# Kernel tuning notes

Measured on AMD Instinct MI355X. Metric: run time of the kernel, lower is better.

Reference implementation:

```python
import jax, jax.numpy as jnp
import numpy as np

EMB = 1024
HEADS = 16
HEAD_DIM = EMB // HEADS
EPS = 1e-5


def gelu_tanh(x):
    c = jnp.sqrt(jnp.asarray(2.0 / jnp.pi, x.dtype))
    return 0.5 * x * (1.0 + jnp.tanh(c * (x + 0.044715 * x ** 3)))


def layernorm(x, scale, shift):
    mean = jnp.mean(x, axis=-1, keepdims=True)
    var = jnp.mean((x - mean) ** 2, axis=-1, keepdims=True)  # unbiased=False
    return scale * (x - mean) / jnp.sqrt(var + EPS) + shift


def setup_inputs() -> dict:
    key = jax.random.key(0)
    ks = jax.random.split(key, 12)
    d, dff = EMB, 4 * EMB
    sd = 1.0 / np.sqrt(d)
    inp = {
        "x": jax.random.normal(ks[0], (2, 2048, d), jnp.float32),
        "Wq": jax.random.normal(ks[1], (d, d), jnp.float32) * sd,
        "Wk": jax.random.normal(ks[2], (d, d), jnp.float32) * sd,
        "Wv": jax.random.normal(ks[3], (d, d), jnp.float32) * sd,
        "Wo": jax.random.normal(ks[4], (d, d), jnp.float32) * sd,
        "bo": jnp.zeros((d,), jnp.float32),
        "W1": jax.random.normal(ks[5], (d, dff), jnp.float32) * sd,
        "b1": jnp.zeros((dff,), jnp.float32),
        "W2": jax.random.normal(ks[6], (dff, d), jnp.float32) * (1.0 / np.sqrt(dff)),
        "b2": jnp.zeros((d,), jnp.float32),
        "g1": jnp.ones((d,), jnp.float32),
        "s1": jnp.zeros((d,), jnp.float32),
        "g2": jnp.ones((d,), jnp.float32),
        "s2": jnp.zeros((d,), jnp.float32),
    }
    return inp


def attention(x, Wq, Wk, Wv, Wo, bo):
    b, s, d = x.shape
    def heads(W):
        return (x @ W).reshape(b, s, HEADS, HEAD_DIM).transpose(0, 2, 1, 3)  # b h s hd
    q, k, v = heads(Wq), heads(Wk), heads(Wv)
    scores = jnp.einsum("bhqd,bhkd->bhqk", q, k)
    causal = jnp.tril(jnp.ones((s, s), bool))
    scores = jnp.where(causal, scores, -jnp.inf)
    w = jax.nn.softmax(scores / np.sqrt(HEAD_DIM), axis=-1)
    ctx = jnp.einsum("bhqk,bhkd->bqhd", w, v).reshape(b, s, d)
    return ctx @ Wo + bo


def reference(x, Wq, Wk, Wv, Wo, bo, W1, b1, W2, b2, g1, s1, g2, s2):
    h = x + attention(layernorm(x, g1, s1), Wq, Wk, Wv, Wo, bo)
    y = layernorm(h, g2, s2)
    y = gelu_tanh(y @ W1 + b1) @ W2 + b2
    return h + y
```

## Files before the change

kernel.cpp:

```cpp
#include <hip/hip_runtime.h>
#include <hip/hip_bf16.h>
#include <stdint.h>
#include <math.h>

#define EMB   1024
#define DFF   4096
#define HEADS 16
#define HD    64
#define BATCH 2
#define SEQ   2048
#define ROWS  (BATCH * SEQ)

typedef __hip_bfloat16 bf16;
typedef short bf16x8_t __attribute__((ext_vector_type(8)));
typedef float f32x4_t __attribute__((ext_vector_type(4)));

typedef const uint32_t __attribute__((address_space(1)))* gp_t;
typedef uint32_t __attribute__((address_space(3)))* lp_t;

__device__ __forceinline__ void async_copy16(const bf16* g, short* l) {
    __builtin_amdgcn_global_load_lds((gp_t)(const void*)g, (lp_t)(void*)l, 16, 0, 0);
}

__device__ __forceinline__ void wait_lds() {
    __asm__ volatile("" ::: "memory");
    __builtin_amdgcn_s_waitcnt(0xC07F);
    __asm__ volatile("" ::: "memory");
}

__device__ __forceinline__ float gelu_f(float x) {
    float z = 0.7978845608028654f * (x + 0.044715f * x * x * x);
    float e = __builtin_amdgcn_exp2f(z * 2.885390081777927f);
    float t = 1.0f - 2.0f * __builtin_amdgcn_rcpf(e + 1.0f);
    return 0.5f * x * (1.0f + t);
}

__device__ __forceinline__ short bf16_bits(float x) {
    bf16 b = (bf16)x;
    short s;
    __builtin_memcpy(&s, &b, 2);
    return s;
}

__device__ __forceinline__ bf16x8_t load8(const bf16* p) {
    bf16x8_t v;
    __builtin_memcpy(&v, p, 16);
    return v;
}

template<int EPI, int BM>
__global__ __launch_bounds__(256) void gemm_k(
    const bf16* __restrict__ A, const bf16* __restrict__ BT,
    bf16* __restrict__ outB, float* __restrict__ outF,
    const float* __restrict__ bias, const float* __restrict__ resF,
    int N, int K, size_t bStrideZ, size_t cStrideZ)
{
    __shared__ alignas(16) short As[2][BM * 32];
    __shared__ alignas(16) short Bs[2][128 * 32];
    constexpr int AI  = BM / 32;
    constexpr int AIS = BM / 64;
    const int tid  = threadIdx.x;
    const int wave = tid >> 6;
    const int lane = tid & 63;
    const int quad = lane >> 4;
    const int l16  = lane & 15;
    const int m0 = blockIdx.y * BM;
    const int n0 = blockIdx.x * 128;
    const int wm = (wave >> 1) * (BM / 2);
    const int wn = (wave & 1) * 64;

    const bf16* Bz = BT + (size_t)blockIdx.z * bStrideZ;

    const bf16* Ag[AIS]; int aoff[AIS];
    const bf16* Bg[2];   int boff[2];
    #pragma unroll
    for (int i = 0; i < AIS; i++) {
        const int c = i * 256 + tid;
        const int row = c >> 2;
        const int lch = (c & 3) ^ ((row >> 1) & 3);
        Ag[i]   = A + (size_t)(m0 + row) * K + lch * 8;
        aoff[i] = (i * 256 + wave * 64) * 8;
    }
    #pragma unroll
    for (int i = 0; i < 2; i++) {
        const int c = i * 256 + tid;
        const int row = c >> 2;
        const int lch = (c & 3) ^ ((row >> 1) & 3);
        Bg[i]   = Bz + (size_t)(n0 + row) * K + lch * 8;
        boff[i] = (i * 256 + wave * 64) * 8;
    }

    f32x4_t acc[AI][4] = {};

    #pragma unroll
    for (int i = 0; i < AIS; i++) async_copy16(Ag[i], &As[0][aoff[i]]);
    #pragma unroll
    for (int i = 0; i < 2; i++)   async_copy16(Bg[i], &Bs[0][boff[i]]);
    __syncthreads();

    int cur = 0;
    for (int k0 = 0; k0 < K; k0 += 32) {
        const int kn = k0 + 32;
        if (kn < K) {
            #pragma unroll
            for (int i = 0; i < AIS; i++) async_copy16(Ag[i] + kn, &As[cur ^ 1][aoff[i]]);
            #pragma unroll
            for (int i = 0; i < 2; i++)   async_copy16(Bg[i] + kn, &Bs[cur ^ 1][boff[i]]);
        }
        bf16x8_t a[AI], b[4];
        #pragma unroll
        for (int i = 0; i < AI; i++) {
            const int r = wm + i * 16 + l16;
            a[i] = *(const bf16x8_t*)&As[cur][r * 32 + ((quad ^ ((r >> 1) & 3)) << 3)];
        }
        #pragma unroll
        for (int j = 0; j < 4; j++) {
            const int r = wn + j * 16 + l16;
            b[j] = *(const bf16x8_t*)&Bs[cur][r * 32 + ((quad ^ ((r >> 1) & 3)) << 3)];
        }
        #pragma unroll
        for (int i = 0; i < AI; i++)
            #pragma unroll
            for (int j = 0; j < 4; j++)
                acc[i][j] = __builtin_amdgcn_mfma_f32_16x16x32_bf16(
                    a[i], b[j], acc[i][j], 0, 0, 0);
        __syncthreads();
        cur ^= 1;
    }

    bf16* outBz = (EPI == 0) ? outB + (size_t)blockIdx.z * cStrideZ : outB;
    #pragma unroll
    for (int j = 0; j < 4; j++) {
        const int col = n0 + wn + j * 16 + l16;
        float bv = 0.0f;
        if constexpr (EPI != 0) bv = bias[col];
        #pragma unroll
        for (int i = 0; i < AI; i++) {
            #pragma unroll
            for (int r = 0; r < 4; r++) {
                const int row = m0 + wm + i * 16 + quad * 4 + r;
                float v = acc[i][j][r] + bv;
                if constexpr (EPI == 1 || EPI == 3) {
                    v += resF[(size_t)row * N + col];
                    outF[(size_t)row * N + col] = v;
                } else if constexpr (EPI == 2) {
                    outBz[(size_t)row * N + col] = (bf16)gelu_f(v);
                } else {
                    outBz[(size_t)row * N + col] = (bf16)v;
                }
            }
        }
    }
}

__global__ __launch_bounds__(256) void ln_k(
    const float* __restrict__ x, const float* __restrict__ g,
    const float* __restrict__ s, bf16* __restrict__ out)
{
    const int row = blockIdx.x;
    const int t = threadIdx.x;
    const size_t base = (size_t)row * EMB + t * 4;
    float v[4];
    #pragma unroll
    for (int e = 0; e < 4; e++) v[e] = x[base + e];
    float sum = v[0] + v[1] + v[2] + v[3];
    float sq  = v[0]*v[0] + v[1]*v[1] + v[2]*v[2] + v[3]*v[3];
    #pragma unroll
    for (int o = 1; o < 64; o <<= 1) {
        sum += __shfl_xor(sum, o);
        sq  += __shfl_xor(sq, o);
    }
    __shared__ float ssum[4], ssq[4];
    const int wave = t >> 6;
    if ((t & 63) == 0) { ssum[wave] = sum; ssq[wave] = sq; }
    __syncthreads();
    sum = ssum[0] + ssum[1] + ssum[2] + ssum[3];
    sq  = ssq[0] + ssq[1] + ssq[2] + ssq[3];
    const float mean = sum * (1.0f / EMB);
    const float var  = sq * (1.0f / EMB) - mean * mean;
    const float rstd = rsqrtf(var + 1e-5f);
    #pragma unroll
    for (int e = 0; e < 4; e++)
        out[base + e] = (bf16)(g[t * 4 + e] * (v[e] - mean) * rstd + s[t * 4 + e]);
}

template<typename T>
__global__ __launch_bounds__(256) void transpose_k(
    const T* __restrict__ src, bf16* __restrict__ dst, int R, int C)
{
    __shared__ bf16 tile[64][65];
    const size_t bo = (size_t)blockIdx.z * R * C;
    const int tx = threadIdx.x, ty = threadIdx.y;
    const int r0 = blockIdx.y * 64, c0 = blockIdx.x * 64;
    #pragma unroll
    for (int i = 0; i < 16; i++) {
        int r = ty + i * 4;
        tile[r][tx] = (bf16)(float)src[bo + (size_t)(r0 + r) * C + c0 + tx];
    }
    __syncthreads();
    #pragma unroll
    for (int i = 0; i < 16; i++) {
        int c = ty + i * 4;
        dst[bo + (size_t)(c0 + c) * R + r0 + tx] = tile[tx][c];
    }
}

__global__ __launch_bounds__(256) void transpose3_k(
    const float* __restrict__ s0, const float* __restrict__ s1,
    const float* __restrict__ s2, bf16* __restrict__ dst, int R, int C)
{
    __shared__ bf16 tile[64][65];
    const float* src = blockIdx.z == 0 ? s0 : (blockIdx.z == 1 ? s1 : s2);
    bf16* d = dst + (size_t)blockIdx.z * R * C;
    const int tx = threadIdx.x, ty = threadIdx.y;
    const int r0 = blockIdx.y * 64, c0 = blockIdx.x * 64;
    #pragma unroll
    for (int i = 0; i < 16; i++) {
        int r = ty + i * 4;
        tile[r][tx] = (bf16)src[(size_t)(r0 + r) * C + c0 + tx];
    }
    __syncthreads();
    #pragma unroll
    for (int i = 0; i < 16; i++) {
        int c = ty + i * 4;
        d[(size_t)(c0 + c) * R + r0 + tx] = tile[tx][c];
    }
}

__global__ __launch_bounds__(256) void attn_k(
    const bf16* __restrict__ q, const bf16* __restrict__ k,
    const bf16* __restrict__ vt, bf16* __restrict__ ctx)
{
    __shared__ alignas(16) short Ks[2][32 * 64];
    __shared__ alignas(16) short Vs[2][64 * 32];
    __shared__ alignas(16) short P[4][16 * 40];
    const int tid = threadIdx.x;
    const int wv = tid >> 6;
    const int lane = tid & 63;
    const int quad = lane >> 4, l16 = lane & 15;

    const int fid = (int)blockIdx.x;
    const int lid = (fid & 7) * 128 + (fid >> 3);
    const int chunk = 31 - (lid & 31);
    const int h = (lid >> 5) & 15;
    const int b = lid >> 9;
    const size_t rowBase = (size_t)b * SEQ;
    const int qb   = chunk * 64 + wv * 16;
    const int nkbw = ((qb + 15) >> 5) + 1;
    const int NK   = chunk * 2 + 2;

    const bf16* kcol  = k + rowBase * EMB + h * HD;
    const bf16* vbase = vt + (size_t)(b * HEADS + h) * HD * SEQ;

    bf16x8_t aq[2];
    #pragma unroll
    for (int s2 = 0; s2 < 2; s2++)
        aq[s2] = load8(&q[(rowBase + qb + l16) * EMB + h * HD + s2 * 32 + quad * 8]);

    f32x4_t O[4] = {};
    float l_p[4] = {};

    const int krow = tid >> 3;
    const int kcc  = (tid & 7) ^ (krow & 7);
    const int vrow = tid >> 2;
    const int vcc  = (tid & 3) ^ (vrow & 3) ^ ((vrow >> 2) & 3);

    async_copy16(kcol + (size_t)krow * EMB + kcc * 8, &Ks[0][wv * 512]);
    async_copy16(vbase + (size_t)vrow * SEQ + vcc * 8, &Vs[0][wv * 512]);
    __syncthreads();

    constexpr float SC = 0.125f * 1.44269504088896f;

    int cur = 0;
    for (int kb = 0; kb < NK; ++kb) {
        const int kbase = kb * 32;
        if (kb + 1 < NK) {
            const int nb = kbase + 32;
            async_copy16(kcol + (size_t)(nb + krow) * EMB + kcc * 8, &Ks[cur ^ 1][wv * 512]);
            async_copy16(vbase + (size_t)vrow * SEQ + nb + vcc * 8, &Vs[cur ^ 1][wv * 512]);
        }
        if (kb < nkbw) {
            bf16x8_t ck[2][2], cv[4];
            #pragma unroll
            for (int nt = 0; nt < 2; nt++) {
                const int kr = nt * 16 + l16;
                #pragma unroll
                for (int s2 = 0; s2 < 2; s2++)
                    ck[nt][s2] = *(const bf16x8_t*)
                        &Ks[cur][kr * 64 + (((s2 * 4 + quad) ^ (kr & 7)) << 3)];
            }
            #pragma unroll
            for (int c = 0; c < 4; c++) {
                const int vr = c * 16 + l16;
                cv[c] = *(const bf16x8_t*)
                    &Vs[cur][vr * 32 + (((quad ^ (vr & 3) ^ ((vr >> 2) & 3))) << 3)];
            }
            f32x4_t sc[2] = {};
            #pragma unroll
            for (int nt = 0; nt < 2; nt++)
                #pragma unroll
                for (int s2 = 0; s2 < 2; s2++)
                    sc[nt] = __builtin_amdgcn_mfma_f32_16x16x32_bf16(
                        aq[s2], ck[nt][s2], sc[nt], 0, 0, 0);
            short* Pw = P[wv];
            if (kbase + 31 <= qb) {
                #pragma unroll
                for (int r = 0; r < 4; r++) {
                    const float p0 = __builtin_amdgcn_exp2f(sc[0][r] * SC);
                    const float p1 = __builtin_amdgcn_exp2f(sc[1][r] * SC);
                    l_p[r] += p0 + p1;
                    Pw[(quad * 4 + r) * 40 + l16]      = bf16_bits(p0);
                    Pw[(quad * 4 + r) * 40 + 16 + l16] = bf16_bits(p1);
                }
            } else {
                #pragma unroll
                for (int r = 0; r < 4; r++) {
                    const int qg = qb + quad * 4 + r;
                    float s0 = sc[0][r] * SC; if (kbase + l16 > qg)      s0 = -1e30f;
                    float s1 = sc[1][r] * SC; if (kbase + 16 + l16 > qg) s1 = -1e30f;
                    const float p0 = __builtin_amdgcn_exp2f(s0);
                    const float p1 = __builtin_amdgcn_exp2f(s1);
                    l_p[r] += p0 + p1;
                    Pw[(quad * 4 + r) * 40 + l16]      = bf16_bits(p0);
                    Pw[(quad * 4 + r) * 40 + 16 + l16] = bf16_bits(p1);
                }
            }
            wait_lds();
            bf16x8_t pa = *(const bf16x8_t*)&Pw[l16 * 40 + quad * 8];
            #pragma unroll
            for (int c = 0; c < 4; c++)
                O[c] = __builtin_amdgcn_mfma_f32_16x16x32_bf16(pa, cv[c], O[c], 0, 0, 0);
        }
        __syncthreads();
        cur ^= 1;
    }

    #pragma unroll
    for (int r = 0; r < 4; r++) {
        float l = l_p[r];
        l += __shfl_xor(l, 1);
        l += __shfl_xor(l, 2);
        l += __shfl_xor(l, 4);
        l += __shfl_xor(l, 8);
        const float inv = 1.0f / l;
        #pragma unroll
        for (int c = 0; c < 4; c++)
            ctx[(rowBase + qb + quad * 4 + r) * EMB + h * HD + c * 16 + l16]
                = (bf16)(O[c][r] * inv);
    }
}

extern "C" void kernel_launch(void* const* d_in, const int* in_sizes, int n_in,
                              void* d_out, int out_size, void* d_ws, size_t ws_size,
                              hipStream_t stream) {
    const float* X  = (const float*)d_in[0];
    const float* Wq = (const float*)d_in[1];
    const float* Wk = (const float*)d_in[2];
    const float* Wv = (const float*)d_in[3];
    const float* Wo = (const float*)d_in[4];
    const float* bo = (const float*)d_in[5];
    const float* W1 = (const float*)d_in[6];
    const float* b1 = (const float*)d_in[7];
    const float* W2 = (const float*)d_in[8];
    const float* b2 = (const float*)d_in[9];
    const float* g1 = (const float*)d_in[10];
    const float* s1 = (const float*)d_in[11];
    const float* g2 = (const float*)d_in[12];
    const float* s2 = (const float*)d_in[13];
    float* out = (float*)d_out;

    char* ws = (char*)d_ws;
    const size_t MB = 1024 * 1024;
    bf16*  lnbuf = (bf16*)(ws + 0);
    bf16*  qkv   = (bf16*)(ws + 8 * MB);
    bf16*  vtb   = (bf16*)(ws + 32 * MB);
    bf16*  ctx   = (bf16*)(ws + 40 * MB);
    float* hbuf  = (float*)(ws + 48 * MB);
    bf16*  WqT   = (bf16*)(ws + 64 * MB);
    bf16*  WoT   = (bf16*)(ws + 70 * MB);
    bf16*  ffn1  = (bf16*)(ws + 8 * MB);
    bf16*  W1T   = (bf16*)(ws + 40 * MB);
    bf16*  W2T   = (bf16*)(ws + 64 * MB);

    const dim3 tb(64, 4);
    transpose3_k<<<dim3(16, 16, 3), tb, 0, stream>>>(Wq, Wk, Wv, WqT, EMB, EMB);
    transpose_k<float><<<dim3(16, 16, 1), tb, 0, stream>>>(Wo, WoT, EMB, EMB);

    ln_k<<<ROWS, 256, 0, stream>>>(X, g1, s1, lnbuf);

    gemm_k<0, 128><<<dim3(8, 32, 3), 256, 0, stream>>>(
        lnbuf, WqT, qkv, nullptr, nullptr, nullptr,
        EMB, EMB, (size_t)EMB * EMB, (size_t)ROWS * EMB);

    transpose_k<bf16><<<dim3(16, 32, BATCH), tb, 0, stream>>>(
        qkv + (size_t)2 * ROWS * EMB, vtb, SEQ, EMB);

    attn_k<<<1024, 256, 0, stream>>>(
        qkv, qkv + (size_t)ROWS * EMB, vtb, ctx);

    gemm_k<1, 64><<<dim3(8, 64), 256, 0, stream>>>(
        ctx, WoT, nullptr, hbuf, bo, X, EMB, EMB, 0, 0);

    transpose_k<float><<<dim3(64, 16, 1), tb, 0, stream>>>(W1, W1T, EMB, DFF);
    transpose_k<float><<<dim3(16, 64, 1), tb, 0, stream>>>(W2, W2T, DFF, EMB);

    ln_k<<<ROWS, 256, 0, stream>>>(hbuf, g2, s2, lnbuf);

    gemm_k<2, 128><<<dim3(32, 32), 256, 0, stream>>>(
        lnbuf, W1T, ffn1, nullptr, b1, nullptr, DFF, EMB, 0, 0);

    gemm_k<3, 64><<<dim3(8, 64), 256, 0, stream>>>(
        ffn1, W2T, nullptr, out, b2, hbuf, EMB, DFF, 0, 0);
}
```

Before: 388.7 us.

## Enlarge attention key/value tile from 32 to 64 keys per iteration

The attention kernel now stages 64-key K and V tiles per loop iteration instead of 32, halving the number of iterations and block-wide barriers. The V layout changes to a 64-wide swizzle, and the P@V product is split into two halves reusing the 32-wide P buffer. The per-wave skip of fully masked key blocks is removed, so waves can compute masked tiles on the diagonal block, and the larger double-buffered shared memory may reduce occupancy.

```diff
diff --git a/kernel.cpp b/kernel.cpp
--- a/kernel.cpp
+++ b/kernel.cpp
@@ -231,8 +231,8 @@
     const bf16* __restrict__ q, const bf16* __restrict__ k,
     const bf16* __restrict__ vt, bf16* __restrict__ ctx)
 {
-    __shared__ alignas(16) short Ks[2][32 * 64];
-    __shared__ alignas(16) short Vs[2][64 * 32];
+    __shared__ alignas(16) short Ks[2][64 * 64];
+    __shared__ alignas(16) short Vs[2][64 * 64];
     __shared__ alignas(16) short P[4][16 * 40];
     const int tid = threadIdx.x;
     const int wv = tid >> 6;
@@ -245,9 +245,8 @@
     const int h = (lid >> 5) & 15;
     const int b = lid >> 9;
     const size_t rowBase = (size_t)b * SEQ;
-    const int qb   = chunk * 64 + wv * 16;
-    const int nkbw = ((qb + 15) >> 5) + 1;
-    const int NK   = chunk * 2 + 2;
+    const int qb = chunk * 64 + wv * 16;
+    const int NK = chunk + 1;
 
     const bf16* kcol  = k + rowBase * EMB + h * HD;
     const bf16* vbase = vt + (size_t)(b * HEADS + h) * HD * SEQ;
@@ -260,69 +259,90 @@
     f32x4_t O[4] = {};
     float l_p[4] = {};
 
-    const int krow = tid >> 3;
-    const int kcc  = (tid & 7) ^ (krow & 7);
-    const int vrow = tid >> 2;
-    const int vcc  = (tid & 3) ^ (vrow & 3) ^ ((vrow >> 2) & 3);
-
-    async_copy16(kcol + (size_t)krow * EMB + kcc * 8, &Ks[0][wv * 512]);
-    async_copy16(vbase + (size_t)vrow * SEQ + vcc * 8, &Vs[0][wv * 512]);
+    int krw[2], kgc[2];
+    #pragma unroll
+    for (int i = 0; i < 2; i++) {
+        const int c = i * 256 + tid;
+        krw[i] = c >> 3;
+        kgc[i] = (c & 7) ^ (krw[i] & 7);
+    }
+    const int ldsOff[2] = { (0 * 256 + wv * 64) * 8, (1 * 256 + wv * 64) * 8 };
+
+    #pragma unroll
+    for (int i = 0; i < 2; i++) {
+        async_copy16(kcol + (size_t)krw[i] * EMB + kgc[i] * 8, &Ks[0][ldsOff[i]]);
+        async_copy16(vbase + (size_t)krw[i] * SEQ + kgc[i] * 8, &Vs[0][ldsOff[i]]);
+    }
     __syncthreads();
 
     constexpr float SC = 0.125f * 1.44269504088896f;
 
     int cur = 0;
     for (int kb = 0; kb < NK; ++kb) {
-        const int kbase = kb * 32;
+        const int kbase = kb * 64;
         if (kb + 1 < NK) {
-            const int nb = kbase + 32;
-            async_copy16(kcol + (size_t)(nb + krow) * EMB + kcc * 8, &Ks[cur ^ 1][wv * 512]);
-            async_copy16(vbase + (size_t)vrow * SEQ + nb + vcc * 8, &Vs[cur ^ 1][wv * 512]);
-        }
-        if (kb < nkbw) {
-            bf16x8_t ck[2][2], cv[4];
-            #pragma unroll
-            for (int nt = 0; nt < 2; nt++) {
-                const int kr = nt * 16 + l16;
-                #pragma unroll
-                for (int s2 = 0; s2 < 2; s2++)
-                    ck[nt][s2] = *(const bf16x8_t*)
-                        &Ks[cur][kr * 64 + (((s2 * 4 + quad) ^ (kr & 7)) << 3)];
+            const int nb = kbase + 64;
+            #pragma unroll
+            for (int i = 0; i < 2; i++) {
+                async_copy16(kcol + (size_t)(nb + krw[i]) * EMB + kgc[i] * 8,
+                             &Ks[cur ^ 1][ldsOff[i]]);
+                async_copy16(vbase + (size_t)krw[i] * SEQ + nb + kgc[i] * 8,
+                             &Vs[cur ^ 1][ldsOff[i]]);
             }
+        }
+        bf16x8_t ck[4][2];
+        #pragma unroll
+        for (int nt = 0; nt < 4; nt++) {
+            const int kr = nt * 16 + l16;
+            #pragma unroll
+            for (int s2 = 0; s2 < 2; s2++)
+                ck[nt][s2] = *(const bf16x8_t*)
+                    &Ks[cur][kr * 64 + (((s2 * 4 + quad) ^ (kr & 7)) << 3)];
+        }
+        f32x4_t sc[4] = {};
+        #pragma unroll
+        for (int nt = 0; nt < 4; nt++)
+            #pragma unroll
+            for (int s2 = 0; s2 < 2; s2++)
+                sc[nt] = __builtin_amdgcn_mfma_f32_16x16x32_bf16(
+                    aq[s2], ck[nt][s2], sc[nt], 0, 0, 0);
+
+        short* Pw = P[wv];
+        const bool full = (kbase + 63 <= qb);
+        #pragma unroll
+        for (int hf = 0; hf < 2; hf++) {
+            bf16x8_t cv[4];
             #pragma unroll
             for (int c = 0; c < 4; c++) {
                 const int vr = c * 16 + l16;
                 cv[c] = *(const bf16x8_t*)
-                    &Vs[cur][vr * 32 + (((quad ^ (vr & 3) ^ ((vr >> 2) & 3))) << 3)];
+                    &Vs[cur][vr * 64 + (((hf * 4 + quad) ^ (vr & 7)) << 3)];
             }
-            f32x4_t sc[2] = {};
-            #pragma unroll
-            for (int nt = 0; nt < 2; nt++)
+            if (full) {
                 #pragma unroll
-                for (int s2 = 0; s2 < 2; s2++)
-                    sc[nt] = __builtin_amdgcn_mfma_f32_16x16x32_bf16(
-                        aq[s2], ck[nt][s2], sc[nt], 0, 0, 0);
-            short* Pw = P[wv];
-            if (kbase + 31 <= qb) {
-                #pragma unroll
-                for (int r = 0; r < 4; r++) {
-                    const float p0 = __builtin_amdgcn_exp2f(sc[0][r] * SC);
-                    const float p1 = __builtin_amdgcn_exp2f(sc[1][r] * SC);
-                    l_p[r] += p0 + p1;
-                    Pw[(quad * 4 + r) * 40 + l16]      = bf16_bits(p0);
-                    Pw[(quad * 4 + r) * 40 + 16 + l16] = bf16_bits(p1);
+                for (int nt2 = 0; nt2 < 2; nt2++) {
+                    const int nt = hf * 2 + nt2;
+                    #pragma unroll
+                    for (int r = 0; r < 4; r++) {
+                        const float p = __builtin_amdgcn_exp2f(sc[nt][r] * SC);
+                        l_p[r] += p;
+                        Pw[(quad * 4 + r) * 40 + nt2 * 16 + l16] = bf16_bits(p);
+                    }
                 }
             } else {
                 #pragma unroll
-                for (int r = 0; r < 4; r++) {
-                    const int qg = qb + quad * 4 + r;
-                    float s0 = sc[0][r] * SC; if (kbase + l16 > qg)      s0 = -1e30f;
-                    float s1 = sc[1][r] * SC; if (kbase + 16 + l16 > qg) s1 = -1e30f;
-                    const float p0 = __builtin_amdgcn_exp2f(s0);
-                    const float p1 = __builtin_amdgcn_exp2f(s1);
-                    l_p[r] += p0 + p1;
-                    Pw[(quad * 4 + r) * 40 + l16]      = bf16_bits(p0);
-                    Pw[(quad * 4 + r) * 40 + 16 + l16] = bf16_bits(p1);
+                for (int nt2 = 0; nt2 < 2; nt2++) {
+                    const int nt = hf * 2 + nt2;
+                    const int kk = kbase + nt * 16 + l16;
+                    #pragma unroll
+                    for (int r = 0; r < 4; r++) {
+                        const int qg = qb + quad * 4 + r;
+                        float s = sc[nt][r] * SC;
+                        if (kk > qg) s = -1e30f;
+                        const float p = __builtin_amdgcn_exp2f(s);
+                        l_p[r] += p;
+                        Pw[(quad * 4 + r) * 40 + nt2 * 16 + l16] = bf16_bits(p);
+                    }
                 }
             }
             wait_lds();
```

New measurement: 380.2 us. 1.02x faster.
